# Kernel tuning notes

Measured on AMD Instinct MI355X. Metric: run time of the kernel, lower is better.

## Reference

```python
import jax, jax.numpy as jnp
import numpy as np

MUL0, MUL1, SCALARS_OUT = 16, 16, 128
L0, L1 = MUL0, MUL1 * 3            # 16, 48
PATH_NUMEL = MUL0 * MUL1 * SCALARS_OUT  # 32768 per path, two paths
EPS = 1e-5
# e3nn normalization: irrep_normalization='component' -> alpha = dim(ir_out) = 1;
# path_normalization='element' -> divide by sum over paths to same output of mul1*mul2 = 256+256 = 512.
PATH_COEFF = 1.0 / np.sqrt(512.0)
CG_110 = 1.0 / np.sqrt(3.0)  # wigner_3j(1,1,0)[i,j] = delta_ij/sqrt(3) (unit Frobenius norm)


def layer_norm(x, g, b):
    mu = jnp.mean(x, axis=-1, keepdims=True)
    var = jnp.mean(jnp.square(x - mu), axis=-1, keepdims=True)
    return (x - mu) * jax.lax.rsqrt(var + EPS) * g + b


def ff_block(x, g, b, w1, w2, b2):
    # LayerNorm -> Linear(no bias) -> SiLU -> Linear(bias); residual=False in both uses
    h = jax.nn.silu(layer_norm(x, g, b) @ w1)
    return h @ w2 + b2


def setup_inputs() -> dict:
    key = jax.random.key(0)
    ks = jax.random.split(key, 8)
    N = 2048
    return {
        "x": jax.random.normal(ks[0], (N, L0 + L1), dtype=jnp.float32),
        "we_ln_g": jnp.ones((L0,), jnp.float32),
        "we_ln_b": jnp.zeros((L0,), jnp.float32),
        "we_w1": jax.random.normal(ks[1], (L0, 4 * L0), jnp.float32) / np.sqrt(L0),
        "we_w2": jax.random.normal(ks[2], (4 * L0, 2 * PATH_NUMEL), jnp.float32) / np.sqrt(4 * L0),
        "we_b2": jnp.zeros((2 * PATH_NUMEL,), jnp.float32),
        "om_ln_g": jnp.ones((SCALARS_OUT,), jnp.float32),
        "om_ln_b": jnp.zeros((SCALARS_OUT,), jnp.float32),
        "om_w1": jax.random.normal(ks[3], (SCALARS_OUT, 4 * SCALARS_OUT), jnp.float32) / np.sqrt(SCALARS_OUT),
        "om_w2": jax.random.normal(ks[4], (4 * SCALARS_OUT, 1), jnp.float32) / np.sqrt(4 * SCALARS_OUT),
        "om_b2": jnp.zeros((1,), jnp.float32),
    }


def reference(x, we_ln_g, we_ln_b, we_w1, we_w2, we_b2,
              om_ln_g, om_ln_b, om_w1, om_w2, om_b2):
    N = x.shape[0]
    feats = x[:, :L0]                       # [N, 16] scalars (0e)
    x1 = x[:, L0:].reshape(N, MUL1, 3)      # [N, 16, 3] vectors (1o)

    # per-sample tensor-product weights (shared_weights=False)
    w = ff_block(feats, we_ln_g, we_ln_b, we_w1, we_w2, we_b2)  # [N, 65536]
    w0 = w[:, :PATH_NUMEL].reshape(N, MUL0, MUL0, SCALARS_OUT)
    w1 = w[:, PATH_NUMEL:].reshape(N, MUL1, MUL1, SCALARS_OUT)

    # path 0: 0e x 0e -> 0e  (uvw)
    o0 = jnp.einsum('nu,nv,nuvw->nw', feats, feats, w0)
    # path 1: 1o x 1o -> 0e  (uvw, CG = delta_ij/sqrt(3))
    o1 = jnp.einsum('nui,nvi,nuvw->nw', x1, x1, w1) * CG_110
    tp_out = PATH_COEFF * (o0 + o1)          # [N, 128]

    return ff_block(tp_out, om_ln_g, om_ln_b, om_w1, om_w2, om_b2)  # [N, 1]
```

## Files before the change

### kernel.cpp

```cpp
#include <hip/hip_runtime.h>
#include <hip/hip_bf16.h>
#include <cstdint>

#define EPS 1e-5f
#define PATH_COEFF 0.04419417382415922f
#define CG110     0.5773502691896258f

typedef __bf16 v8bf __attribute__((ext_vector_type(8)));
typedef float  v4f  __attribute__((ext_vector_type(4)));
typedef _Float16 v4h __attribute__((ext_vector_type(4)));

static __device__ __forceinline__ unsigned short f2bf(float x){
    unsigned int u = __builtin_bit_cast(unsigned int, x);
    u += 0x7fffu + ((u >> 16) & 1u);
    return (unsigned short)(u >> 16);
}
static __device__ __forceinline__ unsigned short f2h(float x){
    return __builtin_bit_cast(unsigned short, (_Float16)x);
}

__global__ __launch_bounds__(256)
void k_pre(const float* __restrict__ w2, const float* __restrict__ b2,
           unsigned short* __restrict__ Vt2,
           const float* __restrict__ om_w1, unsigned short* __restrict__ w1t,
           const float* __restrict__ x, const float* __restrict__ lng,
           const float* __restrict__ lnb, const float* __restrict__ we_w1,
           unsigned short* __restrict__ Q2, float* __restrict__ Ht, int N)
{
    __shared__ __align__(16) unsigned short tile[32][128];
    int b = blockIdx.x;
    int t = threadIdx.x;

    if (b < 260){
        int k    = b >> 2;
        int slab = b & 3;
        const float* srcbase = (k < 64) ? (w2 + (size_t)k * 65536) : b2;
        for (int chunk = 0; chunk < 4; ++chunk){
            int pbase = slab*128 + chunk*32;
            #pragma unroll
            for (int i = 0; i < 4; ++i){
                int g = t + 256*i;
                int ploc = g >> 5, c4 = g & 31;
                const float4 v = *(const float4*)(srcbase + (size_t)(pbase + ploc)*128 + c4*4);
                unsigned int w0 = (unsigned)f2bf(v.x) | ((unsigned)f2bf(v.y) << 16);
                unsigned int w1 = (unsigned)f2bf(v.z) | ((unsigned)f2bf(v.w) << 16);
                *(uint2*)&tile[ploc][c4*4] = make_uint2(w0, w1);
            }
            __syncthreads();
            int w = t & 127, h = t >> 7;
            int ps = slab*4 + chunk;
            unsigned int words[8];
            #pragma unroll
            for (int g2 = 0; g2 < 8; ++g2)
                words[g2] = (unsigned)tile[h*16 + g2*2][w] | ((unsigned)tile[h*16 + g2*2 + 1][w] << 16);
            unsigned short* dq0 = Vt2 + (((size_t)(k*16 + ps)*4 + 2*h    )*128 + w)*8;
            unsigned short* dq1 = Vt2 + (((size_t)(k*16 + ps)*4 + 2*h + 1)*128 + w)*8;
            *(uint4*)dq0 = make_uint4(words[0], words[1], words[2], words[3]);
            *(uint4*)dq1 = make_uint4(words[4], words[5], words[6], words[7]);
            __syncthreads();
        }
    } else if (b < 264){
        int j0 = (b - 260) * 128;
        for (int chunk = 0; chunk < 4; ++chunk){
            #pragma unroll
            for (int i = 0; i < 4; ++i){
                int g = t + 256*i;
                int wloc = g >> 5, c4 = g & 31;
                int w = chunk*32 + wloc;
                const float4 v = *(const float4*)(om_w1 + (size_t)w*512 + j0 + c4*4);
                unsigned int a = (unsigned)f2bf(v.x) | ((unsigned)f2bf(v.y) << 16);
                unsigned int bb = (unsigned)f2bf(v.z) | ((unsigned)f2bf(v.w) << 16);
                *(uint2*)&tile[wloc][c4*4] = make_uint2(a, bb);
            }
            __syncthreads();
            int jl = t & 127, h = t >> 7;
            unsigned int words[8];
            #pragma unroll
            for (int g2 = 0; g2 < 8; ++g2)
                words[g2] = (unsigned)tile[h*16 + g2*2][jl] | ((unsigned)tile[h*16 + g2*2 + 1][jl] << 16);
            unsigned short* dst = w1t + (size_t)(j0 + jl)*128 + chunk*32 + h*16;
            *(uint4*)dst       = make_uint4(words[0], words[1], words[2], words[3]);
            *(uint4*)(dst + 8) = make_uint4(words[4], words[5], words[6], words[7]);
            __syncthreads();
        }
    } else {
        int wv = t >> 6, lane = t & 63;
        int row = (b - 264)*4 + wv;
        const float* xr = x + (size_t)row * 64;
        float f[16]; float mu = 0.f;
        #pragma unroll
        for (int u = 0; u < 16; ++u){ f[u] = xr[u]; mu += f[u]; }
        mu *= (1.f/16.f);
        float var = 0.f;
        #pragma unroll
        for (int u = 0; u < 16; ++u){ float d = f[u] - mu; var += d*d; }
        var *= (1.f/16.f);
        float inv = rsqrtf(var + EPS);
        float lnf[16];
        #pragma unroll
        for (int u = 0; u < 16; ++u) lnf[u] = (f[u]-mu)*inv*lng[u] + lnb[u];
        float h1 = 0.f;
        #pragma unroll
        for (int u = 0; u < 16; ++u) h1 += lnf[u] * we_w1[u*64 + lane];
        float h = h1 / (1.f + expf(-h1));
        Ht[(size_t)lane * N + row] = h;
        if (lane == 0) Ht[(size_t)64 * N + row] = 1.f;

        union { unsigned short qs[8]; uint4 v; } qu;
        #pragma unroll
        for (int j = 0; j < 8; ++j){
            int p = lane*8 + j;
            float q;
            if (p < 256){
                int u = p >> 4, v = p & 15;
                q = PATH_COEFF * f[u] * f[v];
            } else {
                int pp = p - 256;
                int u = pp >> 4, v = pp & 15;
                const float* ya = xr + 16 + u*3;
                const float* yb = xr + 16 + v*3;
                q = (PATH_COEFF * CG110) * (ya[0]*yb[0] + ya[1]*yb[1] + ya[2]*yb[2]);
            }
            qu.qs[j] = f2bf(q);
        }
        int rb = row >> 6, r64 = row & 63;
        int ps = lane >> 2, quad4 = lane & 3;
        *(uint4*)(Q2 + (((size_t)(rb*16 + ps)*4 + quad4)*64 + r64)*8) = qu.v;
    }
}

__global__ __launch_bounds__(256, 4)
void k_main(const unsigned short* __restrict__ Q2, const unsigned short* __restrict__ Vt2,
            const float* __restrict__ Ht, unsigned short* __restrict__ partial, int N)
{
    __shared__ __align__(16) unsigned short stile[4][64*72];
    int g = blockIdx.x & 7;
    int j = blockIdx.x >> 3;
    int kb, mb;
    if (j < 128){ mb = j >> 3; kb = g*8 + (j & 7); }
    else { if (g != 0) return; mb = j - 128; kb = 64; }

    int tid  = threadIdx.x;
    int lane = tid & 63, wv = tid >> 6;
    int r2 = wv >> 1, c2 = wv & 1;
    int quad = lane >> 4, l16 = lane & 15;
    int rowbase = mb*128 + r2*64;
    int rb = rowbase >> 6;
    int wbase = c2*64;

    const unsigned short* aroot = Q2  + (size_t)rb*32768 + quad*512  + l16*8;
    const unsigned short* broot = Vt2 + (size_t)kb*65536 + quad*1024 + (wbase + l16)*8;

    v4f acc[4][4];
    #pragma unroll
    for (int m=0;m<4;++m)
      #pragma unroll
      for (int n=0;n<4;++n)
        #pragma unroll
        for (int r=0;r<4;++r) acc[m][n][r] = 0.f;

    #pragma unroll 4
    for (int ps = 0; ps < 16; ++ps){
        const unsigned short* ap = aroot + ps*2048;
        const unsigned short* bp = broot + ps*4096;
        v8bf a[4], bb[4];
        #pragma unroll
        for (int m=0;m<4;++m) a[m]  = *(const v8bf*)(ap + m*128);
        #pragma unroll
        for (int n=0;n<4;++n) bb[n] = *(const v8bf*)(bp + n*128);
        #pragma unroll
        for (int m=0;m<4;++m)
          #pragma unroll
          for (int n=0;n<4;++n)
            acc[m][n] = __builtin_amdgcn_mfma_f32_16x16x32_bf16(a[m], bb[n], acc[m][n], 0, 0, 0);
    }

    const float* hp = Ht + (size_t)kb*N + rowbase + quad*4;
    unsigned short* my = stile[wv];
    #pragma unroll
    for (int m=0;m<4;++m){
        v4f hv = *(const v4f*)(hp + m*16);
        #pragma unroll
        for (int n=0;n<4;++n)
          #pragma unroll
          for (int r=0;r<4;++r)
            my[(m*16 + quad*4 + r)*72 + n*16 + l16] = f2h(hv[r]*acc[m][n][r]);
    }
    unsigned short* gp = partial + (size_t)kb*N*128 + (size_t)rowbase*128 + wbase;
    #pragma unroll
    for (int i = 0; i < 8; ++i){
        int row = i*8 + (lane >> 3);
        int c16 = (lane & 7)*8;
        uint4 v = *(const uint4*)&my[row*72 + c16];
        *(uint4*)(gp + (size_t)row*128 + c16) = v;
    }
}

__global__ __launch_bounds__(128)
void k_red(const unsigned short* __restrict__ partial, const float* __restrict__ g,
           const float* __restrict__ b, unsigned short* __restrict__ lnf, int N)
{
    int t = threadIdx.x;
    int row0 = blockIdx.x * 4;
    int rl = t >> 5, w = (t & 31)*4;
    int row = row0 + rl;

    const unsigned short* p0 = partial + (size_t)row*128 + w;
    float s0=0.f, s1=0.f, s2=0.f, s3=0.f;
    #pragma unroll
    for (int sl = 0; sl < 65; ++sl){
        v4h v = *(const v4h*)(p0 + (size_t)sl*N*128);
        s0 += (float)v[0]; s1 += (float)v[1]; s2 += (float)v[2]; s3 += (float)v[3];
    }
    float sum = s0+s1+s2+s3;
    float sq  = s0*s0+s1*s1+s2*s2+s3*s3;
    #pragma unroll
    for (int off=16; off>0; off>>=1){
        sum += __shfl_xor(sum, off, 32);
        sq  += __shfl_xor(sq,  off, 32);
    }
    float mu  = sum * (1.f/128.f);
    float var = sq * (1.f/128.f) - mu*mu;
    float inv = rsqrtf(var + EPS);
    unsigned short o[4];
    o[0] = f2bf((s0-mu)*inv*g[w+0] + b[w+0]);
    o[1] = f2bf((s1-mu)*inv*g[w+1] + b[w+1]);
    o[2] = f2bf((s2-mu)*inv*g[w+2] + b[w+2]);
    o[3] = f2bf((s3-mu)*inv*g[w+3] + b[w+3]);
    *(uint2*)(lnf + (size_t)row*128 + w) = *(uint2*)o;
}

__global__ __launch_bounds__(256)
void k_mlp2(const unsigned short* __restrict__ lnf, const unsigned short* __restrict__ w1t,
            const float* __restrict__ w2, const float* __restrict__ b2,
            float* __restrict__ out, int N)
{
    __shared__ float red2[4][64];
    int tid = threadIdx.x, lane = tid & 63, wv = tid >> 6;
    int quad = lane >> 4, l16 = lane & 15;
    int rowbase = blockIdx.x * 64;
    int jbase = wv * 128;

    v4f acc[4][8];
    #pragma unroll
    for (int m=0;m<4;++m)
      #pragma unroll
      for (int n=0;n<8;++n)
        #pragma unroll
        for (int r=0;r<4;++r) acc[m][n][r] = 0.f;

    #pragma unroll
    for (int ps = 0; ps < 4; ++ps){
        v8bf a[4], bb[8];
        #pragma unroll
        for (int m=0;m<4;++m)
            a[m]  = *(const v8bf*)(lnf + (size_t)(rowbase + m*16 + l16)*128 + ps*32 + quad*8);
        #pragma unroll
        for (int n=0;n<8;++n)
            bb[n] = *(const v8bf*)(w1t + (size_t)(jbase + n*16 + l16)*128 + ps*32 + quad*8);
        #pragma unroll
        for (int m=0;m<4;++m)
          #pragma unroll
          for (int n=0;n<8;++n)
            acc[m][n] = __builtin_amdgcn_mfma_f32_16x16x32_bf16(a[m], bb[n], acc[m][n], 0, 0, 0);
    }

    float w2v[8];
    #pragma unroll
    for (int n=0;n<8;++n) w2v[n] = w2[jbase + n*16 + l16];

    #pragma unroll
    for (int m=0;m<4;++m){
        #pragma unroll
        for (int r=0;r<4;++r){
            float s = 0.f;
            #pragma unroll
            for (int n=0;n<8;++n){
                float v = acc[m][n][r];
                s += (v / (1.f + expf(-v))) * w2v[n];
            }
            #pragma unroll
            for (int off=8; off>0; off>>=1) s += __shfl_xor(s, off, 16);
            if (l16 == 0) red2[wv][m*16 + quad*4 + r] = s;
        }
    }
    __syncthreads();
    if (tid < 64)
        out[rowbase + tid] = red2[0][tid] + red2[1][tid] + red2[2][tid] + red2[3][tid] + b2[0];
}

extern "C" void kernel_launch(void* const* d_in, const int* in_sizes, int n_in,
                              void* d_out, int out_size, void* d_ws, size_t ws_size,
                              hipStream_t stream)
{
    const float* x     = (const float*)d_in[0];
    const float* we_g  = (const float*)d_in[1];
    const float* we_b  = (const float*)d_in[2];
    const float* we_w1 = (const float*)d_in[3];
    const float* we_w2 = (const float*)d_in[4];
    const float* we_b2 = (const float*)d_in[5];
    const float* om_g  = (const float*)d_in[6];
    const float* om_b  = (const float*)d_in[7];
    const float* om_w1 = (const float*)d_in[8];
    const float* om_w2 = (const float*)d_in[9];
    const float* om_b2 = (const float*)d_in[10];

    int N  = in_sizes[0] / 64;

    char* ws = (char*)d_ws;
    size_t offV = 0;
    size_t szV  = (size_t)65*16*4*128*8*2;
    size_t offQ = offV + szV;
    size_t szQ  = (size_t)N*512*2;
    size_t offH = offQ + szQ;
    size_t szH  = (size_t)65*N*4;
    size_t offP = offH + szH;
    size_t szP  = (size_t)65*N*128*2;
    size_t offL = offP + szP;
    size_t szL  = (size_t)N*128*2;
    size_t offW = offL + szL;

    unsigned short* Vt2 = (unsigned short*)(ws + offV);
    unsigned short* Q2  = (unsigned short*)(ws + offQ);
    float* Ht           = (float*)(ws + offH);
    unsigned short* Par = (unsigned short*)(ws + offP);
    unsigned short* Lnf = (unsigned short*)(ws + offL);
    unsigned short* W1t = (unsigned short*)(ws + offW);
    float* out = (float*)d_out;

    hipLaunchKernelGGL(k_pre,  dim3(264 + N/4), dim3(256), 0, stream,
                       we_w2, we_b2, Vt2, om_w1, W1t, x, we_g, we_b, we_w1, Q2, Ht, N);
    hipLaunchKernelGGL(k_main, dim3(144*8),     dim3(256), 0, stream, Q2, Vt2, Ht, Par, N);
    hipLaunchKernelGGL(k_red,  dim3(N/4),       dim3(128), 0, stream, Par, om_g, om_b, Lnf, N);
    hipLaunchKernelGGL(k_mlp2, dim3(N/64),      dim3(256), 0, stream, Lnf, W1t, om_w2, om_b2, out, N);
}
```

Measured before the change: 144.8 us.

## Reorganize partial-sum layout by row block and widen reduction loads

```diff
diff --git a/kernel.cpp b/kernel.cpp
--- a/kernel.cpp
+++ b/kernel.cpp
@@ -186,7 +186,8 @@
           for (int r=0;r<4;++r)
             my[(m*16 + quad*4 + r)*72 + n*16 + l16] = f2h(hv[r]*acc[m][n][r]);
     }
-    unsigned short* gp = partial + (size_t)kb*N*128 + (size_t)rowbase*128 + wbase;
+    unsigned short* gp = partial + ((size_t)(mb*65 + kb))*16384
+                                 + (size_t)(r2*64)*128 + wbase;
     #pragma unroll
     for (int i = 0; i < 8; ++i){
         int row = i*8 + (lane >> 3);
@@ -201,33 +202,40 @@
            const float* __restrict__ b, unsigned short* __restrict__ lnf, int N)
 {
     int t = threadIdx.x;
-    int row0 = blockIdx.x * 4;
-    int rl = t >> 5, w = (t & 31)*4;
-    int row = row0 + rl;
-
-    const unsigned short* p0 = partial + (size_t)row*128 + w;
-    float s0=0.f, s1=0.f, s2=0.f, s3=0.f;
-    #pragma unroll
+    int row = blockIdx.x * 8 + (t >> 4);
+    int w8  = (t & 15) * 8;
+    int mb  = row >> 7, rin = row & 127;
+
+    const unsigned short* p0 = partial + (size_t)mb*65*16384 + (size_t)rin*128 + w8;
+
+    float s[8];
+    #pragma unroll
+    for (int j = 0; j < 8; ++j) s[j] = 0.f;
+
+    #pragma unroll 13
     for (int sl = 0; sl < 65; ++sl){
-        v4h v = *(const v4h*)(p0 + (size_t)sl*N*128);
-        s0 += (float)v[0]; s1 += (float)v[1]; s2 += (float)v[2]; s3 += (float)v[3];
-    }
-    float sum = s0+s1+s2+s3;
-    float sq  = s0*s0+s1*s1+s2*s2+s3*s3;
-    #pragma unroll
-    for (int off=16; off>0; off>>=1){
-        sum += __shfl_xor(sum, off, 32);
-        sq  += __shfl_xor(sq,  off, 32);
+        uint4 raw = *(const uint4*)(p0 + (size_t)sl*16384);
+        union { uint4 u; _Float16 h[8]; } cv; cv.u = raw;
+        #pragma unroll
+        for (int j = 0; j < 8; ++j) s[j] += (float)cv.h[j];
+    }
+
+    float sum = 0.f, sq = 0.f;
+    #pragma unroll
+    for (int j = 0; j < 8; ++j){ sum += s[j]; sq += s[j]*s[j]; }
+    #pragma unroll
+    for (int off = 8; off > 0; off >>= 1){
+        sum += __shfl_xor(sum, off, 16);
+        sq  += __shfl_xor(sq,  off, 16);
     }
     float mu  = sum * (1.f/128.f);
     float var = sq * (1.f/128.f) - mu*mu;
     float inv = rsqrtf(var + EPS);
-    unsigned short o[4];
-    o[0] = f2bf((s0-mu)*inv*g[w+0] + b[w+0]);
-    o[1] = f2bf((s1-mu)*inv*g[w+1] + b[w+1]);
-    o[2] = f2bf((s2-mu)*inv*g[w+2] + b[w+2]);
-    o[3] = f2bf((s3-mu)*inv*g[w+3] + b[w+3]);
-    *(uint2*)(lnf + (size_t)row*128 + w) = *(uint2*)o;
+    unsigned short o[8];
+    #pragma unroll
+    for (int j = 0; j < 8; ++j)
+        o[j] = f2bf((s[j]-mu)*inv*g[w8+j] + b[w8+j]);
+    *(uint4*)(lnf + (size_t)row*128 + w8) = *(uint4*)o;
 }
 
 __global__ __launch_bounds__(256)
@@ -235,15 +243,15 @@
             const float* __restrict__ w2, const float* __restrict__ b2,
             float* __restrict__ out, int N)
 {
-    __shared__ float red2[4][64];
+    __shared__ float red2[4][32];
     int tid = threadIdx.x, lane = tid & 63, wv = tid >> 6;
     int quad = lane >> 4, l16 = lane & 15;
-    int rowbase = blockIdx.x * 64;
+    int rowbase = blockIdx.x * 32;
     int jbase = wv * 128;
 
-    v4f acc[4][8];
-    #pragma unroll
-    for (int m=0;m<4;++m)
+    v4f acc[2][8];
+    #pragma unroll
+    for (int m=0;m<2;++m)
       #pragma unroll
       for (int n=0;n<8;++n)
         #pragma unroll
@@ -251,15 +259,15 @@
 
     #pragma unroll
     for (int ps = 0; ps < 4; ++ps){
-        v8bf a[4], bb[8];
-        #pragma unroll
-        for (int m=0;m<4;++m)
+        v8bf a[2], bb[8];
+        #pragma unroll
+        for (int m=0;m<2;++m)
             a[m]  = *(const v8bf*)(lnf + (size_t)(rowbase + m*16 + l16)*128 + ps*32 + quad*8);
         #pragma unroll
         for (int n=0;n<8;++n)
             bb[n] = *(const v8bf*)(w1t + (size_t)(jbase + n*16 + l16)*128 + ps*32 + quad*8);
         #pragma unroll
-        for (int m=0;m<4;++m)
+        for (int m=0;m<2;++m)
           #pragma unroll
           for (int n=0;n<8;++n)
             acc[m][n] = __builtin_amdgcn_mfma_f32_16x16x32_bf16(a[m], bb[n], acc[m][n], 0, 0, 0);
@@ -270,7 +278,7 @@
     for (int n=0;n<8;++n) w2v[n] = w2[jbase + n*16 + l16];
 
     #pragma unroll
-    for (int m=0;m<4;++m){
+    for (int m=0;m<2;++m){
         #pragma unroll
         for (int r=0;r<4;++r){
             float s = 0.f;
@@ -285,7 +293,7 @@
         }
     }
     __syncthreads();
-    if (tid < 64)
+    if (tid < 32)
         out[rowbase + tid] = red2[0][tid] + red2[1][tid] + red2[2][tid] + red2[3][tid] + b2[0];
 }
 
@@ -331,6 +339,6 @@
     hipLaunchKernelGGL(k_pre,  dim3(264 + N/4), dim3(256), 0, stream,
                        we_w2, we_b2, Vt2, om_w1, W1t, x, we_g, we_b, we_w1, Q2, Ht, N);
     hipLaunchKernelGGL(k_main, dim3(144*8),     dim3(256), 0, stream, Q2, Vt2, Ht, Par, N);
-    hipLaunchKernelGGL(k_red,  dim3(N/4),       dim3(128), 0, stream, Par, om_g, om_b, Lnf, N);
-    hipLaunchKernelGGL(k_mlp2, dim3(N/64),      dim3(256), 0, stream, Lnf, W1t, om_w2, om_b2, out, N);
-}
+    hipLaunchKernelGGL(k_red,  dim3(N/8),       dim3(128), 0, stream, Par, om_g, om_b, Lnf, N);
+    hipLaunchKernelGGL(k_mlp2, dim3(N/32),      dim3(256), 0, stream, Lnf, W1t, om_w2, om_b2, out, N);
+}
```

Measured after the change: 137.9 us. -4.8%, faster.
